# Performance work log

Hardware: AMD Instinct MI355X
Metric: run time of the kernel (lower is better)

Reference implementation:

```python
import jax, jax.numpy as jnp
import numpy as np

H, R, B = 8192, 4, 64


def glorot(key, shape):
    return jax.random.uniform(key, shape, minval=-1.0, maxval=1.0) * jnp.sqrt(2.0 / sum(shape))


def setup_inputs() -> dict:
    key = jax.random.key(0)
    k1, k2, k3, k4, kh, kx = jax.random.split(key, 6)
    return {
        "h": jax.random.normal(kh, (B, H), dtype=jnp.float32),
        "x": jax.random.normal(kx, (B, H), dtype=jnp.float32),
        "a_diag": glorot(k1, (H,)).astype(jnp.float32),
        "p_vec": glorot(k2, (H, R)).astype(jnp.float32),
        "q_vec": glorot(k3, (H, R)).astype(jnp.float32),
        "b_mat": glorot(k4, (H, H)).astype(jnp.float32),
    }


def reference(h, x, a_diag, p_vec, q_vec, b_mat):
    # Faithful to the source: explicitly materialize the dense DPLR matrix
    # a_dplr = diag(a_diag) + p q^T  (H x H), then a_dplr @ h + b_mat.T @ x.
    a_dplr = jnp.diag(a_diag) + p_vec @ q_vec.T  # (H, H)
    # Batched over leading dim: (a_dplr @ h_i) == h @ a_dplr.T ; (b_mat.T @ x_i) == x @ b_mat
    return h @ a_dplr.T + x @ b_mat  # (B, H)
```

## Files before the change

### kernel.cpp

```cpp
#include <hip/hip_runtime.h>
#include <hip/hip_bf16.h>


#define HDIM 8192
#define BDIM 64
#define RDIM 4
#define KSPLIT 16
#define KSLAB 512
#define JGRP 256
#define NKSTEP (KSLAB / 32)

typedef short short8 __attribute__((ext_vector_type(8)));
typedef float f32x4 __attribute__((ext_vector_type(4)));
typedef float f32x16 __attribute__((ext_vector_type(16)));

__device__ __forceinline__ unsigned f2bf(float f) {
  unsigned u = __float_as_uint(f);
  unsigned r = u + 0x7fffu + ((u >> 16) & 1u);
  return r >> 16;
}

__device__ __forceinline__ float bf2f(unsigned short u) {
  return __uint_as_float(((unsigned)u) << 16);
}

__global__ __launch_bounds__(256)
void prep_hq_kernel(const float* __restrict__ x,
                    const float* __restrict__ h,
                    const float* __restrict__ q,
                    unsigned short* __restrict__ xb,
                    float* __restrict__ hq) {
  const int b = blockIdx.x, t = threadIdx.x;
  {
    const float* xrow = x + (size_t)b * HDIM;
    unsigned short* xo = xb + (size_t)b * HDIM;
#pragma unroll
    for (int i = 0; i < 4; ++i) {
      const int base = (t * 4 + i) * 8;
      f32x4 v0 = *(const f32x4*)(xrow + base);
      f32x4 v1 = *(const f32x4*)(xrow + base + 4);
      union { unsigned short u[8]; short8 s; } o;
#pragma unroll
      for (int e = 0; e < 4; ++e) {
        o.u[e] = (unsigned short)f2bf(v0[e]);
        o.u[4 + e] = (unsigned short)f2bf(v1[e]);
      }
      *(short8*)(xo + base) = o.s;
    }
  }
  const float* hrow = h + (size_t)b * HDIM;
  f32x4 s = {0.f, 0.f, 0.f, 0.f};
  for (int k = t; k < HDIM; k += 256) {
    float hv = hrow[k];
    f32x4 qv = *(const f32x4*)(q + (size_t)k * RDIM);
    s += hv * qv;
  }
  __shared__ f32x4 red[256];
  red[t] = s;
  __syncthreads();
  for (int off = 128; off > 0; off >>= 1) {
    if (t < off) red[t] += red[t + off];
    __syncthreads();
  }
  if (t == 0) *(f32x4*)(hq + (size_t)b * RDIM) = red[0];
}

__global__ __launch_bounds__(512, 4)
void dplr_main(const float* __restrict__ bmat,
               const unsigned short* __restrict__ xb,
               unsigned short* __restrict__ part) {
  __shared__ __align__(16) unsigned short xs[BDIM * KSLAB];

  const int t    = threadIdx.x;
  const int lane = t & 63;
  const int w    = t >> 6;
  const int c32  = lane & 31;
  const int kh   = lane >> 5;

  const int jg = blockIdx.x & 31;
  const int ks = blockIdx.x >> 5;
  const int k0 = ks * KSLAB;

  {
    const int row = t >> 3;
    const int kq0 = (t & 7) * 8;
    const unsigned short* src = xb + (size_t)row * HDIM + k0 + kq0 * 8;
#pragma unroll
    for (int i = 0; i < 8; ++i) {
      const int g  = row * (KSLAB / 8) + kq0 + i;
      const int gs = g ^ (row & 7);
      *(short8*)&xs[gs * 8] = *(const short8*)(src + i * 8);
    }
  }
  __syncthreads();

  const int j0 = jg * JGRP + w * 32;
  const float* b0 = bmat + (size_t)(k0 + kh * 8) * HDIM + j0 + c32;

  f32x16 acc[2];
#pragma unroll
  for (int mt = 0; mt < 2; ++mt)
#pragma unroll
    for (int r = 0; r < 16; ++r) acc[mt][r] = 0.f;

  float fA[16], fB[16];

  auto issue = [&](int ki, float* g) {
#pragma unroll
    for (int s = 0; s < 2; ++s)
#pragma unroll
      for (int i = 0; i < 8; ++i)
        g[s * 8 + i] = b0[(size_t)(ki * 32 + s * 16 + i) * HDIM];
  };
  auto conv_mfma = [&](int ki, const float* g) {
#pragma unroll
    for (int s = 0; s < 2; ++s) {
      union { unsigned short u[8]; short8 v; } bf;
#pragma unroll
      for (int i = 0; i < 8; ++i) bf.u[i] = (unsigned short)f2bf(g[s * 8 + i]);
#pragma unroll
      for (int mt = 0; mt < 2; ++mt) {
        const int row = mt * 32 + c32;
        const int gg  = row * (KSLAB / 8) + ki * 4 + s * 2 + kh;
        const int gs  = gg ^ (row & 7);
        short8 af = *(const short8*)&xs[gs * 8];
        acc[mt] = __builtin_amdgcn_mfma_f32_32x32x16_bf16(af, bf.v, acc[mt], 0, 0, 0);
      }
    }
  };

  issue(0, fA);
  for (int ki = 0; ki < NKSTEP; ki += 2) {
    issue(ki + 1, fB);
    conv_mfma(ki, fA);
    if (ki + 2 < NKSTEP) issue(ki + 2, fA);
    conv_mfma(ki + 1, fB);
  }

  unsigned short* pb = part + (size_t)ks * BDIM * HDIM;
#pragma unroll
  for (int mt = 0; mt < 2; ++mt)
#pragma unroll
    for (int reg = 0; reg < 16; ++reg) {
      const int row = mt * 32 + (reg & 3) + 8 * (reg >> 2) + 4 * kh;
      const int col = j0 + c32;
      pb[(size_t)row * HDIM + col] = (unsigned short)f2bf(acc[mt][reg]);
    }
}

__global__ __launch_bounds__(256)
void combine_kernel(const unsigned short* __restrict__ part,
                    const float* __restrict__ h,
                    const float* __restrict__ adiag,
                    const float* __restrict__ pvec,
                    const float* __restrict__ hq,
                    float* __restrict__ out) {
  const int tid  = blockIdx.x * 256 + threadIdx.x;
  const int base = tid * 8;
  const int row  = base >> 13;
  const int j    = base & 8191;

  float s[8];
#pragma unroll
  for (int e = 0; e < 8; ++e) s[e] = 0.f;
  const unsigned short* pp = part + (size_t)row * HDIM + j;
#pragma unroll
  for (int ks = 0; ks < KSPLIT; ++ks) {
    union { unsigned short u[8]; short8 v; } pv;
    pv.v = *(const short8*)(pp + (size_t)ks * BDIM * HDIM);
#pragma unroll
    for (int e = 0; e < 8; ++e) s[e] += bf2f(pv.u[e]);
  }
  const f32x4 hv0 = *(const f32x4*)(h + (size_t)row * HDIM + j);
  const f32x4 hv1 = *(const f32x4*)(h + (size_t)row * HDIM + j + 4);
  const f32x4 a0  = *(const f32x4*)(adiag + j);
  const f32x4 a1  = *(const f32x4*)(adiag + j + 4);
  const f32x4 hqv = *(const f32x4*)(hq + (size_t)row * RDIM);

  float res[8];
#pragma unroll
  for (int e = 0; e < 4; ++e) {
    const f32x4 pv = *(const f32x4*)(pvec + (size_t)(j + e) * RDIM);
    res[e] = s[e] + hv0[e] * a0[e] +
             hqv[0] * pv[0] + hqv[1] * pv[1] + hqv[2] * pv[2] + hqv[3] * pv[3];
  }
#pragma unroll
  for (int e = 0; e < 4; ++e) {
    const f32x4 pv = *(const f32x4*)(pvec + (size_t)(j + 4 + e) * RDIM);
    res[4 + e] = s[4 + e] + hv1[e] * a1[e] +
                 hqv[0] * pv[0] + hqv[1] * pv[1] + hqv[2] * pv[2] + hqv[3] * pv[3];
  }
  f32x4 o0 = {res[0], res[1], res[2], res[3]};
  f32x4 o1 = {res[4], res[5], res[6], res[7]};
  *(f32x4*)(out + (size_t)row * HDIM + j) = o0;
  *(f32x4*)(out + (size_t)row * HDIM + j + 4) = o1;
}

extern "C" void kernel_launch(void* const* d_in, const int* in_sizes, int n_in,
                              void* d_out, int out_size, void* d_ws, size_t ws_size,
                              hipStream_t stream) {
  const float* h     = (const float*)d_in[0];
  const float* x     = (const float*)d_in[1];
  const float* adiag = (const float*)d_in[2];
  const float* pvec  = (const float*)d_in[3];
  const float* qvec  = (const float*)d_in[4];
  const float* bmat  = (const float*)d_in[5];
  float* out = (float*)d_out;

  unsigned short* xb = (unsigned short*)d_ws;
  float* hqbuf = (float*)((char*)d_ws + ((size_t)1 << 20));
  unsigned short* part = (unsigned short*)((char*)d_ws + ((size_t)2 << 20));

  prep_hq_kernel<<<BDIM, 256, 0, stream>>>(x, h, qvec, xb, hqbuf);
  dplr_main<<<KSPLIT * 32, 512, 0, stream>>>(bmat, xb, part);
  combine_kernel<<<(BDIM * HDIM / 8) / 256, 256, 0, stream>>>(part, h, adiag, pvec, hqbuf, out);
}
```

Before: 76.29 us.

## Widen B tiles per wave to 64 columns using permlane32 swap for bf16 operands

Each wave now covers 64 output columns instead of 32. Each lane loads one full 256-byte row segment, so B reads are fully coalesced with 64 contiguous floats per row. v_permlane32_swap rearranges the converted bf16 pairs into the MFMA B-operand layout, and each x fragment read from LDS now feeds two MFMAs. The grid is halved to 256 blocks and the launch-bounds occupancy hint drops to 2, which raises register pressure (two 32-float prefetch buffers plus four accumulators) and reduces parallelism.

```diff
diff --git a/kernel.cpp b/kernel.cpp
--- a/kernel.cpp
+++ b/kernel.cpp
@@ -7,8 +7,7 @@
 #define RDIM 4
 #define KSPLIT 16
 #define KSLAB 512
-#define JGRP 256
-#define NKSTEP (KSLAB / 32)
+#define NKTILE (KSLAB / 32)
 
 typedef short short8 __attribute__((ext_vector_type(8)));
 typedef float f32x4 __attribute__((ext_vector_type(4)));
@@ -65,7 +64,7 @@
   if (t == 0) *(f32x4*)(hq + (size_t)b * RDIM) = red[0];
 }
 
-__global__ __launch_bounds__(512, 4)
+__global__ __launch_bounds__(512, 2)
 void dplr_main(const float* __restrict__ bmat,
                const unsigned short* __restrict__ xb,
                unsigned short* __restrict__ part) {
@@ -77,8 +76,8 @@
   const int c32  = lane & 31;
   const int kh   = lane >> 5;
 
-  const int jg = blockIdx.x & 31;
-  const int ks = blockIdx.x >> 5;
+  const int jg = blockIdx.x & 15;
+  const int ks = blockIdx.x >> 4;
   const int k0 = ks * KSLAB;
 
   {
@@ -94,58 +93,70 @@
   }
   __syncthreads();
 
-  const int j0 = jg * JGRP + w * 32;
-  const float* b0 = bmat + (size_t)(k0 + kh * 8) * HDIM + j0 + c32;
-
-  f32x16 acc[2];
+  const int j0 = jg * 512 + w * 64;
+  const float* b0 = bmat + (size_t)k0 * HDIM + j0 + lane;
+
+  f32x16 acc[2][2];
 #pragma unroll
   for (int mt = 0; mt < 2; ++mt)
 #pragma unroll
-    for (int r = 0; r < 16; ++r) acc[mt][r] = 0.f;
-
-  float fA[16], fB[16];
-
-  auto issue = [&](int ki, float* g) {
-#pragma unroll
-    for (int s = 0; s < 2; ++s)
+    for (int nt = 0; nt < 2; ++nt)
+#pragma unroll
+      for (int r = 0; r < 16; ++r) acc[mt][nt][r] = 0.f;
+
+  float LA[32], LB[32];
+
+  auto issue = [&](int tile, float* buf) {
+#pragma unroll
+    for (int i = 0; i < 32; ++i)
+      buf[i] = b0[(size_t)(tile * 32 + i) * HDIM];
+  };
+
+  auto conv_mfma = [&](int tile, const float* buf) {
+#pragma unroll
+    for (int s = 0; s < 2; ++s) {
+      unsigned wv[8];
 #pragma unroll
       for (int i = 0; i < 8; ++i)
-        g[s * 8 + i] = b0[(size_t)(ki * 32 + s * 16 + i) * HDIM];
-  };
-  auto conv_mfma = [&](int ki, const float* g) {
-#pragma unroll
-    for (int s = 0; s < 2; ++s) {
-      union { unsigned short u[8]; short8 v; } bf;
-#pragma unroll
-      for (int i = 0; i < 8; ++i) bf.u[i] = (unsigned short)f2bf(g[s * 8 + i]);
+        wv[i] = f2bf(buf[s * 16 + 2 * i]) | (f2bf(buf[s * 16 + 2 * i + 1]) << 16);
+#pragma unroll
+      for (int j = 0; j < 4; ++j)
+        asm volatile("v_permlane32_swap_b32 %0, %1"
+                     : "+v"(wv[j]), "+v"(wv[4 + j]));
+      union { unsigned u[4]; short8 v; } bf0, bf1;
+#pragma unroll
+      for (int j = 0; j < 4; ++j) { bf0.u[j] = wv[j]; bf1.u[j] = wv[4 + j]; }
 #pragma unroll
       for (int mt = 0; mt < 2; ++mt) {
         const int row = mt * 32 + c32;
-        const int gg  = row * (KSLAB / 8) + ki * 4 + s * 2 + kh;
+        const int gg  = row * (KSLAB / 8) + tile * 4 + s * 2 + kh;
         const int gs  = gg ^ (row & 7);
         short8 af = *(const short8*)&xs[gs * 8];
-        acc[mt] = __builtin_amdgcn_mfma_f32_32x32x16_bf16(af, bf.v, acc[mt], 0, 0, 0);
+        acc[mt][0] = __builtin_amdgcn_mfma_f32_32x32x16_bf16(af, bf0.v, acc[mt][0], 0, 0, 0);
+        acc[mt][1] = __builtin_amdgcn_mfma_f32_32x32x16_bf16(af, bf1.v, acc[mt][1], 0, 0, 0);
       }
     }
   };
 
-  issue(0, fA);
-  for (int ki = 0; ki < NKSTEP; ki += 2) {
-    issue(ki + 1, fB);
-    conv_mfma(ki, fA);
-    if (ki + 2 < NKSTEP) issue(ki + 2, fA);
-    conv_mfma(ki + 1, fB);
+  issue(0, LA);
+  for (int tile = 0; tile < NKTILE; tile += 2) {
+    issue(tile + 1, LB);
+    conv_mfma(tile, LA);
+    if (tile + 2 < NKTILE) issue(tile + 2, LA);
+    conv_mfma(tile + 1, LB);
   }
 
   unsigned short* pb = part + (size_t)ks * BDIM * HDIM;
 #pragma unroll
   for (int mt = 0; mt < 2; ++mt)
 #pragma unroll
-    for (int reg = 0; reg < 16; ++reg) {
-      const int row = mt * 32 + (reg & 3) + 8 * (reg >> 2) + 4 * kh;
-      const int col = j0 + c32;
-      pb[(size_t)row * HDIM + col] = (unsigned short)f2bf(acc[mt][reg]);
-    }
+    for (int nt = 0; nt < 2; ++nt)
+#pragma unroll
+      for (int reg = 0; reg < 16; ++reg) {
+        const int row = mt * 32 + (reg & 3) + 8 * (reg >> 2) + 4 * kh;
+        const int col = j0 + nt * 32 + c32;
+        pb[(size_t)row * HDIM + col] = (unsigned short)f2bf(acc[mt][nt][reg]);
+      }
 }
 
 __global__ __launch_bounds__(256)
@@ -212,6 +223,6 @@
   unsigned short* part = (unsigned short*)((char*)d_ws + ((size_t)2 << 20));
 
   prep_hq_kernel<<<BDIM, 256, 0, stream>>>(x, h, qvec, xb, hqbuf);
-  dplr_main<<<KSPLIT * 32, 512, 0, stream>>>(bmat, xb, part);
+  dplr_main<<<KSPLIT * 16, 512, 0, stream>>>(bmat, xb, part);
   combine_kernel<<<(BDIM * HDIM / 8) / 256, 256, 0, stream>>>(part, h, adiag, pvec, hqbuf, out);
 }
```

Result: faster. 73.21 us (-4.0%).
